# Performance work log

Measured on AMD Instinct MI355X. Metric: run time of the kernel, lower is better.

Reference implementation:

```python
import jax, jax.numpy as jnp
import numpy as np

B = 32768      # batch of ODE state evaluations
N = 64         # input_size (number of variables / per-node MLPs)
H = 64         # hidden_size
N_DISCRETE = 16  # first 16 variables use straight-through gating
HIDDEN_FLAG = True


def setup_inputs() -> dict:
    key = jax.random.key(0)
    k1, k2, k3 = jax.random.split(key, 3)
    inputs = jax.random.normal(k1, (B, N), jnp.float32)
    # Stacked per-node MLP weights: net_i is Linear(N,H,bias=False) -> ReLU -> Linear(H,1,bias=False)
    W1 = jax.random.normal(k2, (N, H, N), jnp.float32) / np.sqrt(N).astype(np.float32)
    W2 = jax.random.normal(k3, (N, H), jnp.float32) / np.sqrt(H).astype(np.float32)
    adjacency = jnp.ones((N, N), jnp.float32)  # buffer, initialized to ones
    discrete_mask = jnp.arange(N) < N_DISCRETE  # bool [N], from input_type_list
    return {"t": 0, "inputs": inputs, "W1": W1, "W2": W2,
            "adjacency": adjacency, "discrete_mask": discrete_mask}


def reference(t, inputs, W1, W2, adjacency, discrete_mask):
    # Straight-through discrete gating: y_hard - sg(y_soft) + y_soft
    y_soft = jax.nn.sigmoid(inputs)
    st = (inputs > 0).astype(inputs.dtype) - jax.lax.stop_gradient(y_soft) + y_soft
    x = jnp.where(discrete_mask[None, :], st, inputs)  # [B, N]

    # Effective per-node input mask: row i of adjacency; last node additionally
    # filtered to only its own (hidden) feature when hidden_flag is set.
    M = adjacency
    if HIDDEN_FLAG:
        one_hot_last = jnp.zeros((N,), M.dtype).at[-1].set(1.0)
        M = M.at[-1].set(M[-1] * one_hot_last)

    # Masking the input of node i by M[i] is equivalent to masking W1[i]'s input dim.
    W1m = W1 * M[:, None, :]                      # [N, H, N]
    h = jax.nn.relu(jnp.einsum('bn,ihn->bih', x, W1m))  # [B, N, H]
    out = jnp.einsum('bih,ih->bi', h, W2)               # [B, N]
    return out
```

## Files before the change

### kernel.cpp

```cpp
#include <hip/hip_runtime.h>
#include <stdint.h>


typedef __attribute__((ext_vector_type(8))) short short8;
typedef __attribute__((ext_vector_type(4))) float floatx4;

#define NN 64
#define HH 64
#define BB 32768
#define LDSW 20
#define X_ELEMS (BB * NN)
#define W1_ELEMS (NN * HH * NN)

__device__ __forceinline__ unsigned short f32_to_bf16_bits(float f) {
    union { float f; unsigned int i; } c; c.f = f;
    unsigned int b = c.i;
    b += 0x7fffu + ((b >> 16) & 1u);
    return (unsigned short)(b >> 16);
}

__device__ __forceinline__ bool sniff_bf16(const void* x) {
    const int lane = threadIdx.x & 63;
    const ushort* xw = (const ushort*)x;
    const ushort a = xw[4 * lane];
    const ushort b = xw[4 * lane + 2];
    const int ea = (a >> 7) & 0xFF, eb = (b >> 7) & 0xFF;
    const int hit = ((ea >= 118 && ea <= 132) ? 1 : 0) + ((eb >= 118 && eb <= 132) ? 1 : 0);
    const unsigned long long m1 = __ballot(hit >= 1);
    const unsigned long long m2 = __ballot(hit >= 2);
    return (__popcll(m1) + __popcll(m2)) >= 64;
}

__global__ __launch_bounds__(256, 4)
void prep_kernel(const void* __restrict__ x, const void* __restrict__ w1,
                 ushort* __restrict__ xo, ushort* __restrict__ w1o)
{
    const bool is_bf16 = sniff_bf16(x);
    const long base = ((long)blockIdx.x * 256 + (long)threadIdx.x) * 8;

    if (base < X_ELEMS) {
        const bool gate = (base & 63) < 16;
        short8 v;
        if (is_bf16) {
            v = *(const short8*)((const ushort*)x + base);
            if (gate) {
                #pragma unroll
                for (int j = 0; j < 8; ++j) {
                    const unsigned short u = (unsigned short)v[j];
                    const bool pos = ((u & 0x8000u) == 0) && ((u & 0x7fffu) != 0);
                    v[j] = pos ? (short)0x3F80 : (short)0;
                }
            }
        } else {
            const float* p = (const float*)x + base;
            const float4 f0 = *(const float4*)(p);
            const float4 f1 = *(const float4*)(p + 4);
            const float vals[8] = {f0.x, f0.y, f0.z, f0.w, f1.x, f1.y, f1.z, f1.w};
            #pragma unroll
            for (int j = 0; j < 8; ++j) {
                if (gate) v[j] = (vals[j] > 0.f) ? (short)0x3F80 : (short)0;
                else      v[j] = (short)f32_to_bf16_bits(vals[j]);
            }
        }
        *(short8*)(xo + base) = v;
    } else {
        const long wb = base - X_ELEMS;
        if (wb < W1_ELEMS) {
            short8 v;
            if (is_bf16) {
                v = *(const short8*)((const ushort*)w1 + wb);
            } else {
                const float* p = (const float*)w1 + wb;
                const float4 f0 = *(const float4*)(p);
                const float4 f1 = *(const float4*)(p + 4);
                const float vals[8] = {f0.x, f0.y, f0.z, f0.w, f1.x, f1.y, f1.z, f1.w};
                #pragma unroll
                for (int j = 0; j < 8; ++j) v[j] = (short)f32_to_bf16_bits(vals[j]);
            }
            const int node = (int)(wb >> 12);
            if (node == NN - 1) {
                const int w63 = (int)(wb & 63);
                #pragma unroll
                for (int j = 0; j < 8; ++j)
                    if (w63 + j != NN - 1) v[j] = 0;
            }
            *(short8*)(w1o + wb) = v;
        }
    }
}

template<bool F32>
__device__ __forceinline__ void main_body(const ushort* __restrict__ xo,
                                          const ushort* __restrict__ w1o,
                                          const void* __restrict__ w2p,
                                          void* __restrict__ outp,
                                          float* slab, float* outTile)
{
    const int tid  = threadIdx.x;
    const int wave = tid >> 6;
    const int lane = tid & 63;
    const int quad = lane >> 4;
    const int l16  = lane & 15;

    const int blk  = blockIdx.x;
    const int ng   = blk >> 9;
    const int rbg  = blk & 511;
    const int b0   = rbg * 64;
    const int nbase = ng * 16 + wave * 4;

    short8 afrag[2][4];
    #pragma unroll
    for (int ks = 0; ks < 2; ++ks)
        #pragma unroll
        for (int rt = 0; rt < 4; ++rt)
            afrag[ks][rt] = *(const short8*)(xo + (b0 + rt * 16 + l16) * NN + ks * 32 + quad * 8);

    float w2reg[4][4];
    #pragma unroll
    for (int nl = 0; nl < 4; ++nl) {
        #pragma unroll
        for (int ht = 0; ht < 4; ++ht) {
            const int idx = (nbase + nl) * HH + ht * 16 + l16;
            if (F32) {
                w2reg[nl][ht] = ((const float*)w2p)[idx];
            } else {
                const ushort u = ((const ushort*)w2p)[idx];
                union { unsigned int i; float f; } cv; cv.i = ((unsigned int)u) << 16;
                w2reg[nl][ht] = cv.f;
            }
        }
    }

    short8 bcur[2][4], bnxt[2][4];
    {
        const ushort* w1n = w1o + nbase * (HH * NN);
        #pragma unroll
        for (int ks = 0; ks < 2; ++ks)
            #pragma unroll
            for (int ht = 0; ht < 4; ++ht)
                bcur[ks][ht] = *(const short8*)(w1n + (ht * 16 + l16) * NN + ks * 32 + quad * 8);
    }

    #pragma unroll 1
    for (int nl = 0; nl < 4; ++nl) {
        if (nl < 3) {
            const ushort* w1n = w1o + (nbase + nl + 1) * (HH * NN);
            #pragma unroll
            for (int ks = 0; ks < 2; ++ks)
                #pragma unroll
                for (int ht = 0; ht < 4; ++ht)
                    bnxt[ks][ht] = *(const short8*)(w1n + (ht * 16 + l16) * NN + ks * 32 + quad * 8);
        }

        floatx4 acc[4][4];
        #pragma unroll
        for (int rt = 0; rt < 4; ++rt)
            #pragma unroll
            for (int ht = 0; ht < 4; ++ht)
                acc[rt][ht] = (floatx4){0.f, 0.f, 0.f, 0.f};

        #pragma unroll
        for (int ks = 0; ks < 2; ++ks)
            #pragma unroll
            for (int rt = 0; rt < 4; ++rt)
                #pragma unroll
                for (int ht = 0; ht < 4; ++ht)
                    acc[rt][ht] = __builtin_amdgcn_mfma_f32_16x16x32_bf16(
                        afrag[ks][rt], bcur[ks][ht], acc[rt][ht], 0, 0, 0);

        #pragma unroll
        for (int rt = 0; rt < 4; ++rt) {
            #pragma unroll
            for (int r = 0; r < 4; ++r) {
                float s = 0.f;
                #pragma unroll
                for (int ht = 0; ht < 4; ++ht) {
                    float v = acc[rt][ht][r];
                    v = v > 0.f ? v : 0.f;
                    s = fmaf(v, w2reg[nl][ht], s);
                }
                slab[(rt * 16 + quad * 4 + r) * LDSW + l16] = s;
            }
        }

        const float* rowp = slab + lane * LDSW;
        const float4 v0 = *(const float4*)(rowp + 0);
        const float4 v1 = *(const float4*)(rowp + 4);
        const float4 v2 = *(const float4*)(rowp + 8);
        const float4 v3 = *(const float4*)(rowp + 12);
        const float tot = (((v0.x + v0.y) + (v0.z + v0.w)) + ((v1.x + v1.y) + (v1.z + v1.w)))
                        + (((v2.x + v2.y) + (v2.z + v2.w)) + ((v3.x + v3.y) + (v3.z + v3.w)));

        outTile[lane * LDSW + wave * 4 + nl] = tot;

        if (nl < 3) {
            #pragma unroll
            for (int ks = 0; ks < 2; ++ks)
                #pragma unroll
                for (int ht = 0; ht < 4; ++ht)
                    bcur[ks][ht] = bnxt[ks][ht];
        }
    }

    __syncthreads();

    const int row = tid >> 2;
    const int c   = tid & 3;
    const float4 v = *(const float4*)(outTile + row * LDSW + c * 4);
    const size_t obase = (size_t)(b0 + row) * NN + ng * 16 + c * 4;
    if (F32) {
        *(float4*)((float*)outp + obase) = v;
    } else {
        ushort4 o;
        o.x = f32_to_bf16_bits(v.x); o.y = f32_to_bf16_bits(v.y);
        o.z = f32_to_bf16_bits(v.z); o.w = f32_to_bf16_bits(v.w);
        *(ushort4*)((ushort*)outp + obase) = o;
    }
}

__global__ __launch_bounds__(256, 2)
void main_kernel(const void* __restrict__ xorig,
                 const ushort* __restrict__ xo, const ushort* __restrict__ w1o,
                 const void* __restrict__ w2p, void* __restrict__ outp)
{
    __shared__ float lds[5 * 64 * LDSW];
    const bool is_bf16 = sniff_bf16(xorig);
    float* slab    = &lds[(threadIdx.x >> 6) * 64 * LDSW];
    float* outTile = &lds[4 * 64 * LDSW];
    if (is_bf16) main_body<false>(xo, w1o, w2p, outp, slab, outTile);
    else         main_body<true >(xo, w1o, w2p, outp, slab, outTile);
}

template<bool F32>
__device__ __forceinline__ void run_body_fb(const void* xp, const void* w1p,
                                            const void* w2p, void* outp,
                                            float* myLds)
{
    const int tid  = threadIdx.x;
    const int wave = tid >> 6;
    const int lane = tid & 63;
    const int quad = lane >> 4;
    const int l16  = lane & 15;
    const int blk  = blockIdx.x;
    const int ng   = blk >> 7;
    const int rbg  = blk & 127;
    const int node = ng * 4 + wave;
    const int rowbase = rbg * 256;

    short8 bfrag[2][4];
    #pragma unroll
    for (int ks = 0; ks < 2; ++ks) {
        #pragma unroll
        for (int ht = 0; ht < 4; ++ht) {
            const int h = ht * 16 + l16;
            const int k = ks * 32 + quad * 8;
            short8 v;
            if (F32) {
                const float* p = (const float*)w1p + node * (HH * NN) + h * NN + k;
                const float4 a0 = *(const float4*)(p);
                const float4 a1 = *(const float4*)(p + 4);
                const float vals[8] = {a0.x, a0.y, a0.z, a0.w, a1.x, a1.y, a1.z, a1.w};
                #pragma unroll
                for (int j = 0; j < 8; ++j) v[j] = (short)f32_to_bf16_bits(vals[j]);
            } else {
                v = *(const short8*)((const ushort*)w1p + node * (HH * NN) + h * NN + k);
            }
            if (node == NN - 1) {
                #pragma unroll
                for (int j = 0; j < 8; ++j)
                    if (k + j != NN - 1) v[j] = 0;
            }
            bfrag[ks][ht] = v;
        }
    }

    float w2reg[4];
    #pragma unroll
    for (int ht = 0; ht < 4; ++ht) {
        const int idx = node * HH + ht * 16 + l16;
        if (F32) {
            w2reg[ht] = ((const float*)w2p)[idx];
        } else {
            const ushort u = ((const ushort*)w2p)[idx];
            union { unsigned int i; float f; } cv; cv.i = ((unsigned int)u) << 16;
            w2reg[ht] = cv.f;
        }
    }

    #pragma unroll 1
    for (int it = 0; it < 4; ++it) {
        const int b0 = rowbase + it * 64;
        short8 afrag[2][4];
        #pragma unroll
        for (int ks = 0; ks < 2; ++ks) {
            #pragma unroll
            for (int rt = 0; rt < 4; ++rt) {
                const int rowg = b0 + rt * 16 + l16;
                const int k    = ks * 32 + quad * 8;
                const bool gate = (ks == 0 && quad < 2);
                short8 v;
                if (F32) {
                    const float* p = (const float*)xp + rowg * NN + k;
                    const float4 a0 = *(const float4*)(p);
                    const float4 a1 = *(const float4*)(p + 4);
                    const float vals[8] = {a0.x, a0.y, a0.z, a0.w, a1.x, a1.y, a1.z, a1.w};
                    #pragma unroll
                    for (int j = 0; j < 8; ++j) {
                        if (gate) v[j] = (vals[j] > 0.f) ? (short)0x3F80 : (short)0;
                        else      v[j] = (short)f32_to_bf16_bits(vals[j]);
                    }
                } else {
                    v = *(const short8*)((const ushort*)xp + rowg * NN + k);
                    if (gate) {
                        #pragma unroll
                        for (int j = 0; j < 8; ++j) {
                            const unsigned short u = (unsigned short)v[j];
                            const bool pos = ((u & 0x8000u) == 0) && ((u & 0x7fffu) != 0);
                            v[j] = pos ? (short)0x3F80 : (short)0;
                        }
                    }
                }
                afrag[ks][rt] = v;
            }
        }

        floatx4 acc[4][4];
        #pragma unroll
        for (int rt = 0; rt < 4; ++rt)
            #pragma unroll
            for (int ht = 0; ht < 4; ++ht)
                acc[rt][ht] = (floatx4){0.f, 0.f, 0.f, 0.f};
        #pragma unroll
        for (int ks = 0; ks < 2; ++ks)
            #pragma unroll
            for (int rt = 0; rt < 4; ++rt)
                #pragma unroll
                for (int ht = 0; ht < 4; ++ht)
                    acc[rt][ht] = __builtin_amdgcn_mfma_f32_16x16x32_bf16(
                        afrag[ks][rt], bfrag[ks][ht], acc[rt][ht], 0, 0, 0);

        #pragma unroll
        for (int rt = 0; rt < 4; ++rt) {
            #pragma unroll
            for (int r = 0; r < 4; ++r) {
                float s = 0.f;
                #pragma unroll
                for (int ht = 0; ht < 4; ++ht) {
                    float v = acc[rt][ht][r];
                    v = v > 0.f ? v : 0.f;
                    s = fmaf(v, w2reg[ht], s);
                }
                myLds[(rt * 16 + quad * 4 + r) * LDSW + l16] = s;
            }
        }
        __syncthreads();
        const float* rowp = myLds + lane * LDSW;
        const float4 v0 = *(const float4*)(rowp + 0);
        const float4 v1 = *(const float4*)(rowp + 4);
        const float4 v2 = *(const float4*)(rowp + 8);
        const float4 v3 = *(const float4*)(rowp + 12);
        const float tot = (((v0.x + v0.y) + (v0.z + v0.w)) + ((v1.x + v1.y) + (v1.z + v1.w)))
                        + (((v2.x + v2.y) + (v2.z + v2.w)) + ((v3.x + v3.y) + (v3.z + v3.w)));
        if (F32) ((float*) outp)[(size_t)(b0 + lane) * NN + node] = tot;
        else     ((ushort*)outp)[(size_t)(b0 + lane) * NN + node] = f32_to_bf16_bits(tot);
        __syncthreads();
    }
}

__global__ __launch_bounds__(256, 2)
void fallback_kernel(const void* __restrict__ x, const void* __restrict__ W1,
                     const void* __restrict__ W2, void* __restrict__ out)
{
    __shared__ float lds[4][64 * LDSW];
    const bool is_bf16 = sniff_bf16(x);
    float* myLds = &lds[threadIdx.x >> 6][0];
    if (is_bf16) run_body_fb<false>(x, W1, W2, out, myLds);
    else         run_body_fb<true >(x, W1, W2, out, myLds);
}

extern "C" void kernel_launch(void* const* d_in, const int* in_sizes, int n_in,
                              void* d_out, int out_size, void* d_ws, size_t ws_size,
                              hipStream_t stream) {
    int i_in = -1, i_w1 = -1, i_w2 = -1;
    for (int i = 0; i < n_in; ++i) {
        const int s = in_sizes[i];
        if      (s == BB * NN  && i_in < 0) i_in = i;
        else if (s == NN*HH*NN && i_w1 < 0) i_w1 = i;
        else if (s == NN*HH    && i_w2 < 0) i_w2 = i;
    }
    if (i_in < 0) i_in = (n_in > 1) ? 1 : 0;
    if (i_w1 < 0) i_w1 = i_in + 1;
    if (i_w2 < 0) i_w2 = i_w1 + 1;

    const size_t need = (size_t)(X_ELEMS + W1_ELEMS) * sizeof(ushort);
    if (ws_size >= need) {
        ushort* xo  = (ushort*)d_ws;
        ushort* w1o = xo + X_ELEMS;
        prep_kernel<<<dim3((X_ELEMS + W1_ELEMS) / (256 * 8)), dim3(256), 0, stream>>>(
            d_in[i_in], d_in[i_w1], xo, w1o);
        main_kernel<<<dim3(4 * 512), dim3(256), 0, stream>>>(
            d_in[i_in], xo, w1o, d_in[i_w2], d_out);
    } else {
        fallback_kernel<<<dim3(16 * 128), dim3(256), 0, stream>>>(
            d_in[i_in], d_in[i_w1], d_in[i_w2], d_out);
    }
}
```

Before: 116.2 us.

## Swap MFMA operand roles so hidden reduction uses lane shuffles instead of LDS slab

The MFMA operands are transposed so W1 is the A operand and x the B operand, placing the hidden dimension along the accumulator rows. The W2-weighted reduction over hidden units then happens in registers plus two cross-lane xor shuffles, replacing the per-wave LDS slab write and readback. W2 loads move inside the node loop as vector loads, and LDS shrinks to a single padded output tile. This cuts LDS traffic and LDS footprint, at the cost of extra shuffle instructions and scalar LDS reads for the final store.

New measurement: 118.7 us. +2.1%, slower.

```diff
diff --git a/kernel.cpp b/kernel.cpp
--- a/kernel.cpp
+++ b/kernel.cpp
@@ -8,7 +8,7 @@
 #define NN 64
 #define HH 64
 #define BB 32768
-#define LDSW 20
+#define OTW 17
 #define X_ELEMS (BB * NN)
 #define W1_ELEMS (NN * HH * NN)
 
@@ -94,7 +94,7 @@
                                           const ushort* __restrict__ w1o,
                                           const void* __restrict__ w2p,
                                           void* __restrict__ outp,
-                                          float* slab, float* outTile)
+                                          float* outTile)
 {
     const int tid  = threadIdx.x;
     const int wave = tid >> 6;
@@ -108,97 +108,100 @@
     const int b0   = rbg * 64;
     const int nbase = ng * 16 + wave * 4;
 
-    short8 afrag[2][4];
+    short8 xfrag[2][4];
     #pragma unroll
     for (int ks = 0; ks < 2; ++ks)
         #pragma unroll
-        for (int rt = 0; rt < 4; ++rt)
-            afrag[ks][rt] = *(const short8*)(xo + (b0 + rt * 16 + l16) * NN + ks * 32 + quad * 8);
-
-    float w2reg[4][4];
-    #pragma unroll
-    for (int nl = 0; nl < 4; ++nl) {
-        #pragma unroll
-        for (int ht = 0; ht < 4; ++ht) {
-            const int idx = (nbase + nl) * HH + ht * 16 + l16;
-            if (F32) {
-                w2reg[nl][ht] = ((const float*)w2p)[idx];
-            } else {
-                const ushort u = ((const ushort*)w2p)[idx];
-                union { unsigned int i; float f; } cv; cv.i = ((unsigned int)u) << 16;
-                w2reg[nl][ht] = cv.f;
-            }
-        }
-    }
-
-    short8 bcur[2][4], bnxt[2][4];
+        for (int nt = 0; nt < 4; ++nt)
+            xfrag[ks][nt] = *(const short8*)(xo + (b0 + nt * 16 + l16) * NN + ks * 32 + quad * 8);
+
+    short8 wcur[2][4], wnxt[2][4];
     {
         const ushort* w1n = w1o + nbase * (HH * NN);
         #pragma unroll
         for (int ks = 0; ks < 2; ++ks)
             #pragma unroll
-            for (int ht = 0; ht < 4; ++ht)
-                bcur[ks][ht] = *(const short8*)(w1n + (ht * 16 + l16) * NN + ks * 32 + quad * 8);
+            for (int mt = 0; mt < 4; ++mt)
+                wcur[ks][mt] = *(const short8*)(w1n + (mt * 16 + l16) * NN + ks * 32 + quad * 8);
     }
 
     #pragma unroll 1
     for (int nl = 0; nl < 4; ++nl) {
+        const int node = nbase + nl;
+
         if (nl < 3) {
-            const ushort* w1n = w1o + (nbase + nl + 1) * (HH * NN);
+            const ushort* w1n = w1o + (node + 1) * (HH * NN);
             #pragma unroll
             for (int ks = 0; ks < 2; ++ks)
                 #pragma unroll
-                for (int ht = 0; ht < 4; ++ht)
-                    bnxt[ks][ht] = *(const short8*)(w1n + (ht * 16 + l16) * NN + ks * 32 + quad * 8);
+                for (int mt = 0; mt < 4; ++mt)
+                    wnxt[ks][mt] = *(const short8*)(w1n + (mt * 16 + l16) * NN + ks * 32 + quad * 8);
+        }
+
+        float w2v[4][4];
+        #pragma unroll
+        for (int mt = 0; mt < 4; ++mt) {
+            const int idx = node * HH + mt * 16 + quad * 4;
+            if (F32) {
+                const float4 w = *(const float4*)((const float*)w2p + idx);
+                w2v[mt][0] = w.x; w2v[mt][1] = w.y; w2v[mt][2] = w.z; w2v[mt][3] = w.w;
+            } else {
+                const ushort4 w = *(const ushort4*)((const ushort*)w2p + idx);
+                union { unsigned int i; float f; } c0, c1, c2, c3;
+                c0.i = ((unsigned int)w.x) << 16; c1.i = ((unsigned int)w.y) << 16;
+                c2.i = ((unsigned int)w.z) << 16; c3.i = ((unsigned int)w.w) << 16;
+                w2v[mt][0] = c0.f; w2v[mt][1] = c1.f; w2v[mt][2] = c2.f; w2v[mt][3] = c3.f;
+            }
         }
 
         floatx4 acc[4][4];
         #pragma unroll
-        for (int rt = 0; rt < 4; ++rt)
-            #pragma unroll
-            for (int ht = 0; ht < 4; ++ht)
-                acc[rt][ht] = (floatx4){0.f, 0.f, 0.f, 0.f};
+        for (int mt = 0; mt < 4; ++mt)
+            #pragma unroll
+            for (int nt = 0; nt < 4; ++nt)
+                acc[mt][nt] = (floatx4){0.f, 0.f, 0.f, 0.f};
 
         #pragma unroll
         for (int ks = 0; ks < 2; ++ks)
             #pragma unroll
-            for (int rt = 0; rt < 4; ++rt)
-                #pragma unroll
-                for (int ht = 0; ht < 4; ++ht)
-                    acc[rt][ht] = __builtin_amdgcn_mfma_f32_16x16x32_bf16(
-                        afrag[ks][rt], bcur[ks][ht], acc[rt][ht], 0, 0, 0);
-
-        #pragma unroll
-        for (int rt = 0; rt < 4; ++rt) {
-            #pragma unroll
-            for (int r = 0; r < 4; ++r) {
-                float s = 0.f;
-                #pragma unroll
-                for (int ht = 0; ht < 4; ++ht) {
-                    float v = acc[rt][ht][r];
-                    v = v > 0.f ? v : 0.f;
-                    s = fmaf(v, w2reg[nl][ht], s);
-                }
-                slab[(rt * 16 + quad * 4 + r) * LDSW + l16] = s;
-            }
-        }
-
-        const float* rowp = slab + lane * LDSW;
-        const float4 v0 = *(const float4*)(rowp + 0);
-        const float4 v1 = *(const float4*)(rowp + 4);
-        const float4 v2 = *(const float4*)(rowp + 8);
-        const float4 v3 = *(const float4*)(rowp + 12);
-        const float tot = (((v0.x + v0.y) + (v0.z + v0.w)) + ((v1.x + v1.y) + (v1.z + v1.w)))
-                        + (((v2.x + v2.y) + (v2.z + v2.w)) + ((v3.x + v3.y) + (v3.z + v3.w)));
-
-        outTile[lane * LDSW + wave * 4 + nl] = tot;
+            for (int mt = 0; mt < 4; ++mt)
+                #pragma unroll
+                for (int nt = 0; nt < 4; ++nt)
+                    acc[mt][nt] = __builtin_amdgcn_mfma_f32_16x16x32_bf16(
+                        wcur[ks][mt], xfrag[ks][nt], acc[mt][nt], 0, 0, 0);
+
+        float psum[4];
+        #pragma unroll
+        for (int nt = 0; nt < 4; ++nt) {
+            float s0 = 0.f, s1 = 0.f;
+            #pragma unroll
+            for (int mt = 0; mt < 4; ++mt) {
+                float a0 = acc[mt][nt][0]; a0 = a0 > 0.f ? a0 : 0.f;
+                float a1 = acc[mt][nt][1]; a1 = a1 > 0.f ? a1 : 0.f;
+                float a2 = acc[mt][nt][2]; a2 = a2 > 0.f ? a2 : 0.f;
+                float a3 = acc[mt][nt][3]; a3 = a3 > 0.f ? a3 : 0.f;
+                s0 = fmaf(a0, w2v[mt][0], s0); s1 = fmaf(a1, w2v[mt][1], s1);
+                s0 = fmaf(a2, w2v[mt][2], s0); s1 = fmaf(a3, w2v[mt][3], s1);
+            }
+            psum[nt] = s0 + s1;
+        }
+
+        #pragma unroll
+        for (int nt = 0; nt < 4; ++nt) {
+            psum[nt] += __shfl_xor(psum[nt], 16, 64);
+            psum[nt] += __shfl_xor(psum[nt], 32, 64);
+        }
+
+        const float val = (quad == 0) ? psum[0] : (quad == 1) ? psum[1]
+                         : (quad == 2) ? psum[2] : psum[3];
+        outTile[lane * OTW + wave * 4 + nl] = val;
 
         if (nl < 3) {
             #pragma unroll
             for (int ks = 0; ks < 2; ++ks)
                 #pragma unroll
-                for (int ht = 0; ht < 4; ++ht)
-                    bcur[ks][ht] = bnxt[ks][ht];
+                for (int mt = 0; mt < 4; ++mt)
+                    wcur[ks][mt] = wnxt[ks][mt];
         }
     }
 
@@ -206,7 +209,8 @@
 
     const int row = tid >> 2;
     const int c   = tid & 3;
-    const float4 v = *(const float4*)(outTile + row * LDSW + c * 4);
+    const float* rp = outTile + row * OTW + c * 4;
+    const float4 v = make_float4(rp[0], rp[1], rp[2], rp[3]);
     const size_t obase = (size_t)(b0 + row) * NN + ng * 16 + c * 4;
     if (F32) {
         *(float4*)((float*)outp + obase) = v;
@@ -223,14 +227,13 @@
                  const ushort* __restrict__ xo, const ushort* __restrict__ w1o,
                  const void* __restrict__ w2p, void* __restrict__ outp)
 {
-    __shared__ float lds[5 * 64 * LDSW];
+    __shared__ float outTile[64 * OTW];
     const bool is_bf16 = sniff_bf16(xorig);
-    float* slab    = &lds[(threadIdx.x >> 6) * 64 * LDSW];
-    float* outTile = &lds[4 * 64 * LDSW];
-    if (is_bf16) main_body<false>(xo, w1o, w2p, outp, slab, outTile);
-    else         main_body<true >(xo, w1o, w2p, outp, slab, outTile);
-}
-
+    if (is_bf16) main_body<false>(xo, w1o, w2p, outp, outTile);
+    else         main_body<true >(xo, w1o, w2p, outp, outTile);
+}
+
+#define LDSW 20
 template<bool F32>
 __device__ __forceinline__ void run_body_fb(const void* xp, const void* w1p,
                                             const void* w2p, void* outp,
```
